# Kernel tuning notes

Measured on AMD Instinct MI355X. Metric: run time of the kernel, lower is better.

The kernel has to match this reference:

```python
import jax, jax.numpy as jnp
import numpy as np

N_NODES = 100000
N_EDGES = 600000
IN_FEAT = 128
OUT_FEAT = 128
NUM_RELS = 8
NUM_BASES = 4


def setup_inputs() -> dict:
    key = jax.random.key(0)
    ks = jax.random.split(key, 8)
    h = jax.random.normal(ks[0], (N_NODES, IN_FEAT), dtype=jnp.float32)
    # xavier-ish scale for params
    weight = jax.random.normal(ks[1], (NUM_BASES, IN_FEAT, OUT_FEAT), dtype=jnp.float32) * (1.0 / np.sqrt(IN_FEAT))
    w_comp = jax.random.normal(ks[2], (NUM_RELS, NUM_BASES), dtype=jnp.float32) * (1.0 / np.sqrt(NUM_BASES))
    root_weight = jax.random.normal(ks[3], (IN_FEAT, OUT_FEAT), dtype=jnp.float32) * (1.0 / np.sqrt(IN_FEAT))
    bias = jnp.zeros((OUT_FEAT,), dtype=jnp.float32)
    src = jax.random.randint(ks[4], (N_EDGES,), 0, N_NODES, dtype=jnp.int32)
    dst = jax.random.randint(ks[5], (N_EDGES,), 0, N_NODES, dtype=jnp.int32)
    rel_type = jax.random.randint(ks[6], (N_EDGES,), 0, NUM_RELS, dtype=jnp.int32)
    return {"h": h, "weight": weight, "w_comp": w_comp, "root_weight": root_weight,
            "bias": bias, "src": src, "dst": dst, "rel_type": rel_type}


def reference(h, weight, w_comp, root_weight, bias, src, dst, rel_type):
    # Basis decomposition: W[r] = sum_b w_comp[r,b] * weight[b]
    B, I, O = weight.shape
    R = w_comp.shape[0]
    W = (w_comp @ weight.reshape(B, I * O)).reshape(R, I, O)  # [R, in, out]
    # msg_e = h[src_e] @ W[rel_e]; computed as all-relation projection + gather
    # (avoids materializing [E, in, out] per-edge weights)
    proj = jnp.einsum('ni,rio->nro', h, W)          # [N, R, out]
    msg = proj[src, rel_type]                        # [E, out]
    agg = jax.ops.segment_sum(msg, dst, num_segments=h.shape[0])  # scatter-sum
    out = h @ root_weight + agg + bias
    return jax.nn.relu(out)
```

## Files before the change

kernel.cpp:

```cpp
#include <hip/hip_runtime.h>
#include <hip/hip_bf16.h>

#define N_NODES 100000
#define N_EDGES 600000
#define FEAT 128
#define NUM_RELS 8
#define NUM_BASES 4
#define NBE 2344

#define PREP_CAST 6250
#define PREP_BLDB 320
#define PREP_ZERO 392
#define PREP_GRID (PREP_CAST + PREP_BLDB + PREP_ZERO)

#define SCAN_TILES 98

typedef short bf16x8 __attribute__((ext_vector_type(8)));
typedef float f32x4  __attribute__((ext_vector_type(4)));
typedef float f32x2  __attribute__((ext_vector_type(2)));

__device__ inline short f2bf(float x) {
    __hip_bfloat16 b = __float2bfloat16(x);
    return *reinterpret_cast<short*>(&b);
}


__global__ __launch_bounds__(256) void k_prep(const float* __restrict__ h,
                                              const float* __restrict__ weight,
                                              const float* __restrict__ rw,
                                              short* __restrict__ hb,
                                              short* __restrict__ Bt,
                                              int* __restrict__ cnt,
                                              int* __restrict__ status) {
    int b = blockIdx.x;
    if (b < PREP_CAST) {
        int i = b * 256 + threadIdx.x;
        const float4* h4 = (const float4*)h;
        float4 v0 = h4[2 * i], v1 = h4[2 * i + 1];
        union { short s[8]; bf16x8 v; } u;
        u.s[0] = f2bf(v0.x); u.s[1] = f2bf(v0.y); u.s[2] = f2bf(v0.z); u.s[3] = f2bf(v0.w);
        u.s[4] = f2bf(v1.x); u.s[5] = f2bf(v1.y); u.s[6] = f2bf(v1.z); u.s[7] = f2bf(v1.w);
        ((bf16x8*)hb)[i] = u.v;
    } else if (b < PREP_CAST + PREP_BLDB) {
        int idx = (b - PREP_CAST) * 256 + threadIdx.x;
        int kc = idx >> 14;
        int e  = idx & 16383;
        int o  = e >> 7, ip = e & 127;
        float v = (kc == 0) ? rw[ip * FEAT + o]
                            : weight[(kc - 1) * FEAT * FEAT + ip * FEAT + o];
        int c = ip >> 3, r = ip & 7;
        int L = (o << 4) | ((c + (o >> 3)) & 15);
        Bt[kc * 16384 + L * 8 + r] = f2bf(v);
    } else {
        int i = (b - PREP_CAST - PREP_BLDB) * 256 + threadIdx.x;
        if (i < N_NODES) cnt[i] = 0;
        else if (i - N_NODES < 128) status[i - N_NODES] = 0;
    }
}

__global__ __launch_bounds__(256) void k_hist_dst(const int* __restrict__ dst,
                                                  int* __restrict__ cnt) {
    int i = blockIdx.x * 256 + threadIdx.x;
    if (i < N_EDGES) atomicAdd(&cnt[dst[i]], 1);
}

__global__ __launch_bounds__(256) void k_scan_lb(const int* __restrict__ cnt,
                                                 int* __restrict__ offs,
                                                 int* __restrict__ cursor,
                                                 int* __restrict__ status) {
    __shared__ int wsum[4];
    __shared__ int bcast;
    int bid = blockIdx.x;
    int lane = threadIdx.x & 63, wid = threadIdx.x >> 6;
    const int N4 = N_NODES / 4;
    int i4 = bid * 256 + threadIdx.x;

    const int4* cnt4 = (const int4*)cnt;
    int4 v = (i4 < N4) ? cnt4[i4] : make_int4(0, 0, 0, 0);
    int s = v.x + v.y + v.z + v.w;
    int incl = s;
#pragma unroll
    for (int d = 1; d < 64; d <<= 1) {
        int t = __shfl_up(incl, d);
        if (lane >= d) incl += t;
    }
    if (lane == 63) wsum[wid] = incl;
    __syncthreads();
    if (threadIdx.x == 0) {
        int a = 0;
#pragma unroll
        for (int w = 0; w < 4; ++w) { int x = wsum[w]; wsum[w] = a; a += x; }
        int total = a;
        __hip_atomic_store(&status[bid], (total << 2) | 1,
                           __ATOMIC_RELEASE, __HIP_MEMORY_SCOPE_AGENT);
        int excl = 0;
        for (int t = bid - 1; t >= 0; ) {
            int st = __hip_atomic_load(&status[t],
                                       __ATOMIC_ACQUIRE, __HIP_MEMORY_SCOPE_AGENT);
            if ((st & 3) == 0) { __builtin_amdgcn_s_sleep(1); continue; }
            excl += st >> 2;
            if ((st & 3) == 2) break;
            --t;
        }
        __hip_atomic_store(&status[bid], ((excl + total) << 2) | 2,
                           __ATOMIC_RELEASE, __HIP_MEMORY_SCOPE_AGENT);
        bcast = excl;
        if (bid == SCAN_TILES - 1) offs[N_NODES] = excl + total;
    }
    __syncthreads();
    int base = bcast + wsum[wid] + incl - s;
    if (i4 < N4) {
        int4 ex;
        ex.x = base;
        ex.y = base + v.x;
        ex.z = base + v.x + v.y;
        ex.w = base + v.x + v.y + v.z;
        ((int4*)offs)[i4]   = ex;
        ((int4*)cursor)[i4] = ex;
    }
}

__global__ __launch_bounds__(256) void k_scatter_sorted(const int* __restrict__ src,
                                                        const int* __restrict__ dst,
                                                        const int* __restrict__ rel,
                                                        int* __restrict__ cursor,
                                                        int* __restrict__ packed) {
    int e = blockIdx.x * 256 + threadIdx.x;
    if (e < N_EDGES) {
        int p = atomicAdd(&cursor[dst[e]], 1);
        packed[p] = (src[e] << 3) | rel[e];
    }
}

__global__ __launch_bounds__(256) void k_edge_z(const int* __restrict__ offs,
                                                const int* __restrict__ packed,
                                                const float* __restrict__ wc,
                                                const short* __restrict__ hb,
                                                unsigned int* __restrict__ z_u32) {
    int wid = threadIdx.x >> 6, lane = threadIdx.x & 63;
    int d = blockIdx.x * 4 + wid;
    if (d >= N_NODES) return;
    int s = offs[d], e = offs[d + 1];

    const float4* wc4 = (const float4*)wc;
    const unsigned int* hbu = (const unsigned int*)hb;

    f32x2 z2[4] = {(f32x2)0.f, (f32x2)0.f, (f32x2)0.f, (f32x2)0.f};

    for (int base = s; base < e; base += 64) {
        int rem = e - base;
        int m = rem < 64 ? rem : 64;
        int pk = (lane < m) ? packed[base + lane] : 0;
        int j = 0;
        for (; j + 3 < m; j += 4) {
            int p0 = __builtin_amdgcn_readlane(pk, j);
            int p1 = __builtin_amdgcn_readlane(pk, j + 1);
            int p2 = __builtin_amdgcn_readlane(pk, j + 2);
            int p3 = __builtin_amdgcn_readlane(pk, j + 3);
            unsigned int v0 = hbu[(size_t)(p0 >> 3) * 64 + lane];
            unsigned int v1 = hbu[(size_t)(p1 >> 3) * 64 + lane];
            unsigned int v2 = hbu[(size_t)(p2 >> 3) * 64 + lane];
            unsigned int v3 = hbu[(size_t)(p3 >> 3) * 64 + lane];
            float4 c0 = wc4[p0 & 7];
            float4 c1 = wc4[p1 & 7];
            float4 c2 = wc4[p2 & 7];
            float4 c3 = wc4[p3 & 7];
            f32x2 h0; h0.x = __int_as_float(v0 << 16); h0.y = __int_as_float(v0 & 0xffff0000u);
            f32x2 h1; h1.x = __int_as_float(v1 << 16); h1.y = __int_as_float(v1 & 0xffff0000u);
            f32x2 h2; h2.x = __int_as_float(v2 << 16); h2.y = __int_as_float(v2 & 0xffff0000u);
            f32x2 h3; h3.x = __int_as_float(v3 << 16); h3.y = __int_as_float(v3 & 0xffff0000u);
            f32x2 cc;
            cc = c0.x; z2[0] += cc * h0;
            cc = c0.y; z2[1] += cc * h0;
            cc = c0.z; z2[2] += cc * h0;
            cc = c0.w; z2[3] += cc * h0;
            cc = c1.x; z2[0] += cc * h1;
            cc = c1.y; z2[1] += cc * h1;
            cc = c1.z; z2[2] += cc * h1;
            cc = c1.w; z2[3] += cc * h1;
            cc = c2.x; z2[0] += cc * h2;
            cc = c2.y; z2[1] += cc * h2;
            cc = c2.z; z2[2] += cc * h2;
            cc = c2.w; z2[3] += cc * h2;
            cc = c3.x; z2[0] += cc * h3;
            cc = c3.y; z2[1] += cc * h3;
            cc = c3.z; z2[2] += cc * h3;
            cc = c3.w; z2[3] += cc * h3;
        }
        for (; j < m; ++j) {
            int p0 = __builtin_amdgcn_readlane(pk, j);
            unsigned int v0 = hbu[(size_t)(p0 >> 3) * 64 + lane];
            float4 c0 = wc4[p0 & 7];
            f32x2 h0; h0.x = __int_as_float(v0 << 16); h0.y = __int_as_float(v0 & 0xffff0000u);
            f32x2 cc;
            cc = c0.x; z2[0] += cc * h0;
            cc = c0.y; z2[1] += cc * h0;
            cc = c0.z; z2[2] += cc * h0;
            cc = c0.w; z2[3] += cc * h0;
        }
    }

    unsigned int* row = z_u32 + (size_t)d * 256;
#pragma unroll
    for (int b = 0; b < 4; ++b) {
        unsigned int lo = ((unsigned int)(unsigned short)f2bf(z2[b].x));
        unsigned int hi = ((unsigned int)(unsigned short)f2bf(z2[b].y)) << 16;
        row[b * 64 + lane] = lo | hi;
    }
}

__global__ __launch_bounds__(256) void k_gemm_fused(const short* __restrict__ hb,
                                                    const short* __restrict__ z,
                                                    const short* __restrict__ Bt,
                                                    const float* __restrict__ bias,
                                                    float* __restrict__ out) {
    __shared__ short lds[FEAT * FEAT];
    int wave = threadIdx.x >> 6, lane = threadIdx.x & 63;
    int quad = lane >> 4, n16 = lane & 15;
    int base = blockIdx.x * 64 + wave * 16;

    int rowA = base + n16;
    if (rowA >= N_NODES) rowA = N_NODES - 1;

    f32x4 acc[8];
#pragma unroll
    for (int nt = 0; nt < 8; ++nt) acc[nt] = (f32x4)0.f;

    const bf16x8* bp = (const bf16x8*)lds;
    char* lds_base = (char*)lds;

    for (int kc = 0; kc < 5; ++kc) {
        if (kc) __syncthreads();
        const char* gsrc = (const char*)Bt + kc * 32768;
#pragma unroll
        for (int t = 0; t < 8; ++t) {
            unsigned int off = wave * 8192 + t * 1024;
            __builtin_amdgcn_global_load_lds(
                (const __attribute__((address_space(1))) unsigned int*)(gsrc + off + lane * 16),
                (__attribute__((address_space(3))) unsigned int*)(lds_base + off),
                16, 0, 0);
        }
        __syncthreads();

        const bf16x8* ap = (kc == 0)
            ? (const bf16x8*)(hb + (size_t)rowA * FEAT)
            : (const bf16x8*)(z + (size_t)rowA * 512 + (kc - 1) * FEAT);

#pragma unroll
        for (int ks = 0; ks < 4; ++ks) {
            bf16x8 a = ap[ks * 4 + quad];
            int sw = (ks * 4 + quad + n16) & 15;
#pragma unroll
            for (int nt = 0; nt < 8; ++nt) {
                int o = n16 * 8 + nt;
                bf16x8 b = bp[(o << 4) + sw];
                acc[nt] = __builtin_amdgcn_mfma_f32_16x16x32_bf16(a, b, acc[nt], 0, 0, 0);
            }
        }
    }

    float bv[8];
#pragma unroll
    for (int nt = 0; nt < 8; ++nt) bv[nt] = bias[n16 * 8 + nt];

#pragma unroll
    for (int reg = 0; reg < 4; ++reg) {
        int node = base + quad * 4 + reg;
        if (node < N_NODES) {
            float4 fa, fb;
            fa.x = fmaxf(acc[0][reg] + bv[0], 0.f);
            fa.y = fmaxf(acc[1][reg] + bv[1], 0.f);
            fa.z = fmaxf(acc[2][reg] + bv[2], 0.f);
            fa.w = fmaxf(acc[3][reg] + bv[3], 0.f);
            fb.x = fmaxf(acc[4][reg] + bv[4], 0.f);
            fb.y = fmaxf(acc[5][reg] + bv[5], 0.f);
            fb.z = fmaxf(acc[6][reg] + bv[6], 0.f);
            fb.w = fmaxf(acc[7][reg] + bv[7], 0.f);
            float* row = out + (size_t)node * FEAT + n16 * 8;
            *(float4*)row       = fa;
            *(float4*)(row + 4) = fb;
        }
    }
}


extern "C" void kernel_launch(void* const* d_in, const int* in_sizes, int n_in,
                              void* d_out, int out_size, void* d_ws, size_t ws_size,
                              hipStream_t stream) {
    const float* h    = (const float*)d_in[0];
    const float* wgt  = (const float*)d_in[1];
    const float* wcmp = (const float*)d_in[2];
    const float* rw   = (const float*)d_in[3];
    const float* bias = (const float*)d_in[4];
    const int*   src  = (const int*)d_in[5];
    const int*   dst  = (const int*)d_in[6];
    const int*   rel  = (const int*)d_in[7];
    float* out = (float*)d_out;

    char* ws = (char*)d_ws;
    short*        hb     = (short*)(ws + 0);
    short*        Bt     = (short*)(ws + 25600000ull);
    short*        z      = (short*)(ws + 25763840ull);
    unsigned int* z_u32  = (unsigned int*)z;
    int*          packed = (int*)(ws + 128163840ull);
    int*          cnt    = (int*)(ws + 130563840ull);
    int*          offs   = (int*)(ws + 130963840ull);
    int*          cursor = (int*)(ws + 131363968ull);
    int*          status = (int*)(ws + 131763968ull);

    hipLaunchKernelGGL(k_prep,     dim3(PREP_GRID), dim3(256), 0, stream,
                       h, wgt, rw, hb, Bt, cnt, status);
    hipLaunchKernelGGL(k_hist_dst, dim3(NBE),  dim3(256), 0, stream, dst, cnt);
    hipLaunchKernelGGL(k_scan_lb,  dim3(SCAN_TILES), dim3(256), 0, stream,
                       cnt, offs, cursor, status);
    hipLaunchKernelGGL(k_scatter_sorted, dim3(NBE), dim3(256), 0, stream,
                       src, dst, rel, cursor, packed);
    hipLaunchKernelGGL(k_edge_z,   dim3((N_NODES + 3) / 4), dim3(256), 0, stream,
                       offs, packed, wcmp, hb, z_u32);
    hipLaunchKernelGGL(k_gemm_fused, dim3((N_NODES + 63) / 64), dim3(256), 0, stream,
                       hb, z, Bt, bias, out);
}
```

Baseline: 265.8 us.

## Store B in MFMA fragment order and prefetch next A chunk in fused GEMM

The weight matrix is now prepared in the exact per-lane MFMA fragment order, so each wave reads B from LDS with contiguous lane-indexed loads instead of a swizzled row index. The fused GEMM also loads the next K-chunk's A operand (from z) into registers before computing the current chunk, overlapping global latency with MFMA work. This costs extra registers for the double-buffered A fragments, and the new layout may bring different LDS bank behaviour.

Result: no change. 266.6 us (+0.3%).

```diff
diff --git a/kernel.cpp b/kernel.cpp
--- a/kernel.cpp
+++ b/kernel.cpp
@@ -29,7 +29,7 @@
                                               const float* __restrict__ weight,
                                               const float* __restrict__ rw,
                                               short* __restrict__ hb,
-                                              short* __restrict__ Bt,
+                                              short* __restrict__ Btf,
                                               int* __restrict__ cnt,
                                               int* __restrict__ status) {
     int b = blockIdx.x;
@@ -48,9 +48,10 @@
         int o  = e >> 7, ip = e & 127;
         float v = (kc == 0) ? rw[ip * FEAT + o]
                             : weight[(kc - 1) * FEAT * FEAT + ip * FEAT + o];
-        int c = ip >> 3, r = ip & 7;
-        int L = (o << 4) | ((c + (o >> 3)) & 15);
-        Bt[kc * 16384 + L * 8 + r] = f2bf(v);
+        int nt = o & 7, n16 = o >> 3;
+        int ks = ip >> 5, quad = (ip >> 3) & 3, j = ip & 7;
+        int lane = quad * 16 + n16;
+        Btf[((kc * 4 + ks) * 8 + nt) * 512 + lane * 8 + j] = f2bf(v);
     } else {
         int i = (b - PREP_CAST - PREP_BLDB) * 256 + threadIdx.x;
         if (i < N_NODES) cnt[i] = 0;
@@ -211,7 +212,7 @@
 
 __global__ __launch_bounds__(256) void k_gemm_fused(const short* __restrict__ hb,
                                                     const short* __restrict__ z,
-                                                    const short* __restrict__ Bt,
+                                                    const short* __restrict__ Btf,
                                                     const float* __restrict__ bias,
                                                     float* __restrict__ out) {
     __shared__ short lds[FEAT * FEAT];
@@ -229,9 +230,16 @@
     const bf16x8* bp = (const bf16x8*)lds;
     char* lds_base = (char*)lds;
 
+    bf16x8 a_cur[4];
+    {
+        const bf16x8* ap = (const bf16x8*)(hb + (size_t)rowA * FEAT);
+#pragma unroll
+        for (int ks = 0; ks < 4; ++ks) a_cur[ks] = ap[ks * 4 + quad];
+    }
+
     for (int kc = 0; kc < 5; ++kc) {
         if (kc) __syncthreads();
-        const char* gsrc = (const char*)Bt + kc * 32768;
+        const char* gsrc = (const char*)Btf + kc * 32768;
 #pragma unroll
         for (int t = 0; t < 8; ++t) {
             unsigned int off = wave * 8192 + t * 1024;
@@ -242,20 +250,26 @@
         }
         __syncthreads();
 
-        const bf16x8* ap = (kc == 0)
-            ? (const bf16x8*)(hb + (size_t)rowA * FEAT)
-            : (const bf16x8*)(z + (size_t)rowA * 512 + (kc - 1) * FEAT);
+        bf16x8 a_nxt[4];
+        if (kc < 4) {
+            const bf16x8* ap = (const bf16x8*)(z + (size_t)rowA * 512 + kc * FEAT);
+#pragma unroll
+            for (int ks = 0; ks < 4; ++ks) a_nxt[ks] = ap[ks * 4 + quad];
+        }
 
 #pragma unroll
         for (int ks = 0; ks < 4; ++ks) {
-            bf16x8 a = ap[ks * 4 + quad];
-            int sw = (ks * 4 + quad + n16) & 15;
+            const bf16x8* bks = bp + ks * 512 + lane;
 #pragma unroll
             for (int nt = 0; nt < 8; ++nt) {
-                int o = n16 * 8 + nt;
-                bf16x8 b = bp[(o << 4) + sw];
-                acc[nt] = __builtin_amdgcn_mfma_f32_16x16x32_bf16(a, b, acc[nt], 0, 0, 0);
+                bf16x8 b = bks[nt * 64];
+                acc[nt] = __builtin_amdgcn_mfma_f32_16x16x32_bf16(a_cur[ks], b, acc[nt], 0, 0, 0);
             }
+        }
+
+        if (kc < 4) {
+#pragma unroll
+            for (int ks = 0; ks < 4; ++ks) a_cur[ks] = a_nxt[ks];
         }
     }
 
@@ -299,7 +313,7 @@
 
     char* ws = (char*)d_ws;
     short*        hb     = (short*)(ws + 0);
-    short*        Bt     = (short*)(ws + 25600000ull);
+    short*        Btf    = (short*)(ws + 25600000ull);
     short*        z      = (short*)(ws + 25763840ull);
     unsigned int* z_u32  = (unsigned int*)z;
     int*          packed = (int*)(ws + 128163840ull);
@@ -309,7 +323,7 @@
     int*          status = (int*)(ws + 131763968ull);
 
     hipLaunchKernelGGL(k_prep,     dim3(PREP_GRID), dim3(256), 0, stream,
-                       h, wgt, rw, hb, Bt, cnt, status);
+                       h, wgt, rw, hb, Btf, cnt, status);
     hipLaunchKernelGGL(k_hist_dst, dim3(NBE),  dim3(256), 0, stream, dst, cnt);
     hipLaunchKernelGGL(k_scan_lb,  dim3(SCAN_TILES), dim3(256), 0, stream,
                        cnt, offs, cursor, status);
@@ -318,5 +332,5 @@
     hipLaunchKernelGGL(k_edge_z,   dim3((N_NODES + 3) / 4), dim3(256), 0, stream,
                        offs, packed, wcmp, hb, z_u32);
     hipLaunchKernelGGL(k_gemm_fused, dim3((N_NODES + 63) / 64), dim3(256), 0, stream,
-                       hb, z, Bt, bias, out);
-}
+                       hb, z, Btf, bias, out);
+}
```
